# Kernel optimization log

Measured on AMD Instinct MI355X. Metric: run time of the kernel, lower is better.

Reference implementation:

```python
import jax, jax.numpy as jnp
import numpy as np

NUM_STRINGS = 6
WEIGHT_FRET_ONSET = 0.5
STRING_WEIGHTS = jnp.ones((NUM_STRINGS,), dtype=jnp.float32)

B, S, T, C = 64, 6, 2000, 25


def setup_inputs() -> dict:
    key = jax.random.key(0)
    k1, k2, k3, k4 = jax.random.split(key, 4)
    return {
        "output_fret": jax.random.normal(k1, (B, S, T, C), dtype=jnp.float32),
        "target_fret": jax.random.randint(k2, (B, S, T), 0, C),
        "output_onset": jax.random.normal(k3, (B, S, T), dtype=jnp.float32),
        "target_onset": jax.random.uniform(k4, (B, S, T), dtype=jnp.float32),
    }


def reference(output_fret, target_fret, output_onset, target_onset):
    # ---- fret loss: standard CE over classes, mean over batch per (s,t),
    #      summed over frames, weighted per string ----
    logp_fret = jax.nn.log_softmax(output_fret, axis=-1)            # [B,S,T,C]
    nll = -jnp.take_along_axis(logp_fret, target_fret[..., None], axis=-1)[..., 0]  # [B,S,T]
    fret_st = nll.mean(axis=0)                                       # [S,T] (reduction='mean' over batch)
    fret_string_losses = fret_st.sum(axis=1) * STRING_WEIGHTS        # [S]
    fret_loss = fret_string_losses.sum()

    # ---- onset loss: torch CE with 1D [B] input + [B] float target =
    #      single example with B classes and probability targets:
    #      softmax over the BATCH dimension ----
    logp_on = jax.nn.log_softmax(output_onset, axis=0)               # softmax over B
    on_st = -(target_onset * logp_on).sum(axis=0)                    # [S,T]
    onset_string_losses = on_st.sum(axis=1) * STRING_WEIGHTS         # [S]
    onset_loss = onset_string_losses.sum()

    loss = WEIGHT_FRET_ONSET * fret_loss + (1.0 - WEIGHT_FRET_ONSET) * onset_loss
    return (loss, fret_loss, onset_loss, fret_string_losses, onset_string_losses)
```

## Files before the change

### kernel.cpp

```cpp
#include <hip/hip_runtime.h>
#include <math.h>

constexpr int Bn = 64, Sn = 6, Tn = 2000, Cn = 25;
constexpr int COLS = Sn * Tn;
constexpr int ROWS = Bn * Sn * Tn;
constexpr int BDIM = 256;
constexpr int WV   = 4;

constexpr int TROWS = 64;
constexpr int TF4   = TROWS * Cn / 4;
constexpr int NT    = 4;
constexpr int RPW   = NT * TROWS;
constexpr int RPB   = WV * RPW;
constexpr int FBLK  = ROWS / RPB;
constexpr int FPAD  = 768;

constexpr int OCOLS = 64;
constexpr int OBLK  = (COLS + OCOLS - 1) / OCOLS;
constexpr int OPAD  = 192;
constexpr int GRID  = OBLK + FBLK;

typedef const __attribute__((address_space(1))) unsigned int guint;
typedef __attribute__((address_space(3)))       unsigned int luint;

static __device__ __forceinline__ void seg_reduce_add(float* ls, int s, float v, int lane) {
    const int s0 = __shfl(s, 0, 64);
    const int s1 = __shfl(s, 63, 64);
    if (s0 == s1) {
        float a = v;
        #pragma unroll
        for (int off = 32; off; off >>= 1) a += __shfl_xor(a, off, 64);
        if (lane == 0) atomicAdd(&ls[s0], a);
    } else {
        float a = (s == s0) ? v : 0.0f;
        float b = (s == s0) ? 0.0f : v;
        #pragma unroll
        for (int off = 32; off; off >>= 1) {
            a += __shfl_xor(a, off, 64);
            b += __shfl_xor(b, off, 64);
        }
        if (lane == 0) { atomicAdd(&ls[s0], a); atomicAdd(&ls[s1], b); }
    }
}

__global__ __launch_bounds__(BDIM) void main_kernel(const float4* __restrict__ x4,
                                                    const int*    __restrict__ tgt,
                                                    const float*  __restrict__ ox,
                                                    const float*  __restrict__ ot,
                                                    float* __restrict__ pf,
                                                    float* __restrict__ po) {
    __shared__ float4 buf4[WV][2][TF4];
    __shared__ float  ws[WV][Sn];
    const int tid  = threadIdx.x;
    const int lane = tid & 63;
    const int w    = tid >> 6;
    if (lane < Sn) ws[w][lane] = 0.0f;

    if (blockIdx.x < OBLK) {
        const int cb  = blockIdx.x;
        const int col = cb * OCOLS + lane;
        float4* ob4 = &buf4[0][0][0];
        float M = -INFINITY, S = 0.0f, ts = 0.0f, txs = 0.0f;
        if (col < COLS) {
            const int b0 = w * 16;
            #pragma unroll
            for (int h = 0; h < 2; ++h) {
                float xv[8], tv[8];
                #pragma unroll
                for (int k = 0; k < 8; ++k) xv[k] = ox[(b0 + h * 8 + k) * COLS + col];
                #pragma unroll
                for (int k = 0; k < 8; ++k) tv[k] = ot[(b0 + h * 8 + k) * COLS + col];
                float cm = -INFINITY;
                #pragma unroll
                for (int k = 0; k < 8; ++k) cm = fmaxf(cm, xv[k]);
                float cs = 0.0f;
                #pragma unroll
                for (int k = 0; k < 8; ++k) cs += __expf(xv[k] - cm);
                const float nm = fmaxf(M, cm);
                S = S * __expf(M - nm) + cs * __expf(cm - nm);
                M = nm;
                #pragma unroll
                for (int k = 0; k < 8; ++k) { ts += tv[k]; txs += tv[k] * xv[k]; }
            }
        }
        ob4[w * OCOLS + lane] = make_float4(M, S, ts, txs);
        __syncthreads();
        if (tid < OCOLS) {
            float on = 0.0f;
            int   s  = Sn - 1;
            const int c = cb * OCOLS + tid;
            if (c < COLS) {
                s = c / Tn;
                float4 p0 = ob4[0 * OCOLS + tid];
                float Mm = p0.x, Sm = p0.y, tsm = p0.z, txm = p0.w;
                #pragma unroll
                for (int q = 1; q < WV; ++q) {
                    const float4 p = ob4[q * OCOLS + tid];
                    const float nm = fmaxf(Mm, p.x);
                    Sm  = Sm * __expf(Mm - nm) + p.y * __expf(p.x - nm);
                    Mm  = nm;
                    tsm += p.z; txm += p.w;
                }
                on = tsm * (Mm + __logf(Sm)) - txm;
            }
            seg_reduce_add(ws[0], s, on, tid);
            if (tid < Sn) po[tid * OPAD + cb] = ws[0][tid];
        }
    } else {
        const int fb    = blockIdx.x - OBLK;
        const int wrow0 = fb * RPB + w * RPW;
        const float4* gw = x4 + (long)(wrow0 / 4) * Cn;
        float4* bb = &buf4[w][0][0];

        int tcs[NT];
        #pragma unroll
        for (int t = 0; t < NT; ++t) tcs[t] = tgt[wrow0 + t * TROWS + lane];

        auto stage = [&](int t) {
            const int b = t & 1;
            const float4* gs = gw + (long)t * TF4 + lane;
            #pragma unroll
            for (int k = 0; k < 6; ++k)
                __builtin_amdgcn_global_load_lds((guint*)(gs + k * 64),
                                                 (luint*)(bb + b * TF4 + k * 64), 16, 0, 0);
            if (lane < 16)
                __builtin_amdgcn_global_load_lds((guint*)(gs + 384),
                                                 (luint*)(bb + b * TF4 + 384), 16, 0, 0);
        };

        auto compute = [&](int t) {
            const int b  = t & 1;
            const int tc = tcs[t];
            const float* rp = (const float*)(bb + b * TF4) + lane * Cn;
            float m = -INFINITY, xt = 0.0f;
            #pragma unroll
            for (int c = 0; c < Cn; ++c) {
                const float e = rp[c];
                m  = fmaxf(m, e);
                xt = (c == tc) ? e : xt;
            }
            float ss = 0.0f;
            #pragma unroll
            for (int c = 0; c < Cn; ++c) ss += __expf(rp[c] - m);
            const float nll = m + __logf(ss) - xt;
            const int s = ((wrow0 + t * TROWS + lane) / Tn) % Sn;
            seg_reduce_add(ws[w], s, nll, lane);
        };

        stage(0);
        stage(1);
        #pragma unroll
        for (int t = 0; t < NT; ++t) {
            if (t < NT - 1)
                asm volatile("s_waitcnt vmcnt(7)" ::: "memory");
            else
                asm volatile("s_waitcnt vmcnt(0)" ::: "memory");
            compute(t);
            if (t + 2 < NT) {
                asm volatile("s_waitcnt lgkmcnt(0)" ::: "memory");
                stage(t + 2);
            }
        }
        __syncthreads();
        if (tid < Sn)
            pf[tid * FPAD + fb] = ws[0][tid] + ws[1][tid] + ws[2][tid] + ws[3][tid];
    }
}

__global__ __launch_bounds__(1024) void finish_kernel(const float* __restrict__ pf,
                                                      const float* __restrict__ po,
                                                      float* __restrict__ out) {
    __shared__ float acc[2 * Sn];
    const int tid  = threadIdx.x;
    const int lane = tid & 63;
    if (tid < 2 * Sn) acc[tid] = 0.0f;
    __syncthreads();

    float fs[Sn];
    #pragma unroll
    for (int s = 0; s < Sn; ++s) {
        float v = 0.0f;
        for (int i = tid; i < FBLK; i += 1024) v += pf[s * FPAD + i];
        fs[s] = v;
    }
    #pragma unroll
    for (int off = 32; off; off >>= 1) {
        #pragma unroll
        for (int s = 0; s < Sn; ++s) fs[s] += __shfl_xor(fs[s], off, 64);
    }
    if (lane == 0) {
        #pragma unroll
        for (int s = 0; s < Sn; ++s) atomicAdd(&acc[s], fs[s]);
    }

    const int wv = tid >> 6;
    if (wv < Sn) {
        float v = 0.0f;
        for (int i = lane; i < OBLK; i += 64) v += po[wv * OPAD + i];
        #pragma unroll
        for (int off = 32; off; off >>= 1) v += __shfl_xor(v, off, 64);
        if (lane == 0) acc[Sn + wv] = v;
    }
    __syncthreads();

    if (tid == 0) {
        float fret = 0.0f, on = 0.0f, fsv[Sn], osv[Sn];
        #pragma unroll
        for (int s = 0; s < Sn; ++s) {
            fsv[s] = acc[s] * (1.0f / Bn);
            osv[s] = acc[Sn + s];
            fret += fsv[s];
            on   += osv[s];
        }
        out[0] = 0.5f * fret + 0.5f * on;
        out[1] = fret;
        out[2] = on;
        #pragma unroll
        for (int s = 0; s < Sn; ++s) { out[3 + s] = fsv[s]; out[9 + s] = osv[s]; }
    }
}

extern "C" void kernel_launch(void* const* d_in, const int* in_sizes, int n_in,
                              void* d_out, int out_size, void* d_ws, size_t ws_size,
                              hipStream_t stream) {
    const float* output_fret  = (const float*)d_in[0];
    const int*   target_fret  = (const int*)d_in[1];
    const float* output_onset = (const float*)d_in[2];
    const float* target_onset = (const float*)d_in[3];
    float* pf  = (float*)d_ws;
    float* po  = pf + Sn * FPAD;
    float* out = (float*)d_out;

    main_kernel<<<GRID, BDIM, 0, stream>>>((const float4*)output_fret, target_fret,
                                           output_onset, target_onset, pf, po);
    finish_kernel<<<1, 1024, 0, stream>>>(pf, po, out);
}
```

Measured before the change: 25.94 us.

## Fuse finish reduction into main kernel via per-block flags and interleave onset blocks

Removes the second finish kernel launch. An extra last block spins on per-block global completion flags, then reduces the partials and writes the outputs, resetting the flags for the next call. Onset blocks are interleaved among fret blocks (every fifth block) so their work spreads across the grid. The target logit is now read by direct LDS indexing instead of a select inside the loop. The spinning block relies on being scheduled alongside the others and relaxed atomics for visibility, which adds forward-progress and memory-ordering risk.

```diff
diff --git a/kernel.cpp b/kernel.cpp
--- a/kernel.cpp
+++ b/kernel.cpp
@@ -12,16 +12,31 @@
 constexpr int NT    = 4;
 constexpr int RPW   = NT * TROWS;
 constexpr int RPB   = WV * RPW;
-constexpr int FBLK  = ROWS / RPB;
-constexpr int FPAD  = 768;
+constexpr int NFB   = ROWS / RPB;
 
 constexpr int OCOLS = 64;
-constexpr int OBLK  = (COLS + OCOLS - 1) / OCOLS;
-constexpr int OPAD  = 192;
-constexpr int GRID  = OBLK + FBLK;
+constexpr int NOB   = (COLS + OCOLS - 1) / OCOLS;
+constexpr int NBLK  = NFB + NOB;
+constexpr int GRID  = NBLK + 1;
+constexpr int PAD   = 1024;
 
 typedef const __attribute__((address_space(1))) unsigned int guint;
 typedef __attribute__((address_space(3)))       unsigned int luint;
+
+__device__ int g_flag[NBLK];
+
+static __device__ __forceinline__ float agent_loadf(const float* p) {
+    return __hip_atomic_load(p, __ATOMIC_RELAXED, __HIP_MEMORY_SCOPE_AGENT);
+}
+static __device__ __forceinline__ void agent_storef(float* p, float v) {
+    __hip_atomic_store(p, v, __ATOMIC_RELAXED, __HIP_MEMORY_SCOPE_AGENT);
+}
+static __device__ __forceinline__ int agent_loadi(const int* p) {
+    return __hip_atomic_load(p, __ATOMIC_RELAXED, __HIP_MEMORY_SCOPE_AGENT);
+}
+static __device__ __forceinline__ void agent_storei(int* p, int v) {
+    __hip_atomic_store(p, v, __ATOMIC_RELAXED, __HIP_MEMORY_SCOPE_AGENT);
+}
 
 static __device__ __forceinline__ void seg_reduce_add(float* ls, int s, float v, int lane) {
     const int s0 = __shfl(s, 0, 64);
@@ -48,16 +63,77 @@
                                                     const float*  __restrict__ ox,
                                                     const float*  __restrict__ ot,
                                                     float* __restrict__ pf,
-                                                    float* __restrict__ po) {
+                                                    float* __restrict__ po,
+                                                    float* __restrict__ out) {
     __shared__ float4 buf4[WV][2][TF4];
     __shared__ float  ws[WV][Sn];
+    __shared__ float  acc[2 * Sn];
+    __shared__ int    nr;
     const int tid  = threadIdx.x;
     const int lane = tid & 63;
     const int w    = tid >> 6;
+    const int b    = blockIdx.x;
     if (lane < Sn) ws[w][lane] = 0.0f;
 
-    if (blockIdx.x < OBLK) {
-        const int cb  = blockIdx.x;
+    if (b == NBLK) {
+        for (;;) {
+            int ok = 1;
+            for (int i = tid; i < NBLK; i += BDIM) ok &= agent_loadi(&g_flag[i]);
+            if (tid == 0) nr = 0;
+            __syncthreads();
+            if (!ok) nr = 1;
+            __syncthreads();
+            if (nr == 0) break;
+            __builtin_amdgcn_s_sleep(16);
+        }
+        if (tid < 2 * Sn) acc[tid] = 0.0f;
+        __syncthreads();
+        float fs[Sn], os[Sn];
+        #pragma unroll
+        for (int s = 0; s < Sn; ++s) {
+            float v = 0.0f;
+            for (int i = tid; i < NFB; i += BDIM) v += agent_loadf(&pf[s * PAD + i]);
+            fs[s] = v;
+            float u = 0.0f;
+            for (int i = tid; i < NOB; i += BDIM) u += agent_loadf(&po[s * PAD + i]);
+            os[s] = u;
+        }
+        #pragma unroll
+        for (int off = 32; off; off >>= 1) {
+            #pragma unroll
+            for (int s = 0; s < Sn; ++s) {
+                fs[s] += __shfl_xor(fs[s], off, 64);
+                os[s] += __shfl_xor(os[s], off, 64);
+            }
+        }
+        if (lane == 0) {
+            #pragma unroll
+            for (int s = 0; s < Sn; ++s) { atomicAdd(&acc[s], fs[s]); atomicAdd(&acc[Sn + s], os[s]); }
+        }
+        __syncthreads();
+        if (tid == 0) {
+            float fret = 0.0f, on = 0.0f, fsv[Sn], osv[Sn];
+            #pragma unroll
+            for (int s = 0; s < Sn; ++s) {
+                fsv[s] = acc[s] * (1.0f / Bn);
+                osv[s] = acc[Sn + s];
+                fret += fsv[s];
+                on   += osv[s];
+            }
+            out[0] = 0.5f * fret + 0.5f * on;
+            out[1] = fret;
+            out[2] = on;
+            #pragma unroll
+            for (int s = 0; s < Sn; ++s) { out[3 + s] = fsv[s]; out[9 + s] = osv[s]; }
+        }
+        for (int i = tid; i < NBLK; i += BDIM) agent_storei(&g_flag[i], 0);
+        return;
+    }
+
+    const bool isOn = ((b % 5) == 2) && (b / 5 < NOB);
+
+    if (isOn) {
+        const int cb  = b / 5;
         const int col = cb * OCOLS + lane;
         float4* ob4 = &buf4[0][0][0];
         float M = -INFINITY, S = 0.0f, ts = 0.0f, txs = 0.0f;
@@ -104,11 +180,13 @@
                 on = tsm * (Mm + __logf(Sm)) - txm;
             }
             seg_reduce_add(ws[0], s, on, tid);
-            if (tid < Sn) po[tid * OPAD + cb] = ws[0][tid];
+            if (tid < Sn) agent_storef(&po[tid * PAD + cb], ws[0][tid]);
+            asm volatile("s_waitcnt vmcnt(0)" ::: "memory");
+            if (tid == 0) agent_storei(&g_flag[b], 1);
         }
     } else {
-        const int fb    = blockIdx.x - OBLK;
-        const int wrow0 = fb * RPB + w * RPW;
+        const int fid   = b - ((b + 2) / 5 < NOB ? (b + 2) / 5 : NOB);
+        const int wrow0 = fid * RPB + w * RPW;
         const float4* gw = x4 + (long)(wrow0 / 4) * Cn;
         float4* bb = &buf4[w][0][0];
 
@@ -117,28 +195,24 @@
         for (int t = 0; t < NT; ++t) tcs[t] = tgt[wrow0 + t * TROWS + lane];
 
         auto stage = [&](int t) {
-            const int b = t & 1;
+            const int p = t & 1;
             const float4* gs = gw + (long)t * TF4 + lane;
             #pragma unroll
             for (int k = 0; k < 6; ++k)
                 __builtin_amdgcn_global_load_lds((guint*)(gs + k * 64),
-                                                 (luint*)(bb + b * TF4 + k * 64), 16, 0, 0);
+                                                 (luint*)(bb + p * TF4 + k * 64), 16, 0, 0);
             if (lane < 16)
                 __builtin_amdgcn_global_load_lds((guint*)(gs + 384),
-                                                 (luint*)(bb + b * TF4 + 384), 16, 0, 0);
+                                                 (luint*)(bb + p * TF4 + 384), 16, 0, 0);
         };
 
         auto compute = [&](int t) {
-            const int b  = t & 1;
             const int tc = tcs[t];
-            const float* rp = (const float*)(bb + b * TF4) + lane * Cn;
-            float m = -INFINITY, xt = 0.0f;
-            #pragma unroll
-            for (int c = 0; c < Cn; ++c) {
-                const float e = rp[c];
-                m  = fmaxf(m, e);
-                xt = (c == tc) ? e : xt;
-            }
+            const float* rp = (const float*)(bb + (t & 1) * TF4) + lane * Cn;
+            const float xt = rp[tc];
+            float m = -INFINITY;
+            #pragma unroll
+            for (int c = 0; c < Cn; ++c) m = fmaxf(m, rp[c]);
             float ss = 0.0f;
             #pragma unroll
             for (int c = 0; c < Cn; ++c) ss += __expf(rp[c] - m);
@@ -163,60 +237,10 @@
         }
         __syncthreads();
         if (tid < Sn)
-            pf[tid * FPAD + fb] = ws[0][tid] + ws[1][tid] + ws[2][tid] + ws[3][tid];
-    }
-}
-
-__global__ __launch_bounds__(1024) void finish_kernel(const float* __restrict__ pf,
-                                                      const float* __restrict__ po,
-                                                      float* __restrict__ out) {
-    __shared__ float acc[2 * Sn];
-    const int tid  = threadIdx.x;
-    const int lane = tid & 63;
-    if (tid < 2 * Sn) acc[tid] = 0.0f;
-    __syncthreads();
-
-    float fs[Sn];
-    #pragma unroll
-    for (int s = 0; s < Sn; ++s) {
-        float v = 0.0f;
-        for (int i = tid; i < FBLK; i += 1024) v += pf[s * FPAD + i];
-        fs[s] = v;
-    }
-    #pragma unroll
-    for (int off = 32; off; off >>= 1) {
-        #pragma unroll
-        for (int s = 0; s < Sn; ++s) fs[s] += __shfl_xor(fs[s], off, 64);
-    }
-    if (lane == 0) {
-        #pragma unroll
-        for (int s = 0; s < Sn; ++s) atomicAdd(&acc[s], fs[s]);
-    }
-
-    const int wv = tid >> 6;
-    if (wv < Sn) {
-        float v = 0.0f;
-        for (int i = lane; i < OBLK; i += 64) v += po[wv * OPAD + i];
-        #pragma unroll
-        for (int off = 32; off; off >>= 1) v += __shfl_xor(v, off, 64);
-        if (lane == 0) acc[Sn + wv] = v;
-    }
-    __syncthreads();
-
-    if (tid == 0) {
-        float fret = 0.0f, on = 0.0f, fsv[Sn], osv[Sn];
-        #pragma unroll
-        for (int s = 0; s < Sn; ++s) {
-            fsv[s] = acc[s] * (1.0f / Bn);
-            osv[s] = acc[Sn + s];
-            fret += fsv[s];
-            on   += osv[s];
-        }
-        out[0] = 0.5f * fret + 0.5f * on;
-        out[1] = fret;
-        out[2] = on;
-        #pragma unroll
-        for (int s = 0; s < Sn; ++s) { out[3 + s] = fsv[s]; out[9 + s] = osv[s]; }
+            agent_storef(&pf[tid * PAD + fid],
+                         ws[0][tid] + ws[1][tid] + ws[2][tid] + ws[3][tid]);
+        asm volatile("s_waitcnt vmcnt(0)" ::: "memory");
+        if (tid == 0) agent_storei(&g_flag[b], 1);
     }
 }
 
@@ -228,10 +252,9 @@
     const float* output_onset = (const float*)d_in[2];
     const float* target_onset = (const float*)d_in[3];
     float* pf  = (float*)d_ws;
-    float* po  = pf + Sn * FPAD;
+    float* po  = pf + Sn * PAD;
     float* out = (float*)d_out;
 
     main_kernel<<<GRID, BDIM, 0, stream>>>((const float4*)output_fret, target_fret,
-                                           output_onset, target_onset, pf, po);
-    finish_kernel<<<1, 1024, 0, stream>>>(pf, po, out);
-}
+                                           output_onset, target_onset, pf, po, out);
+}
```

New measurement: 31.20 us. 20.3% more time.

## Replace static fret tile assignment with atomic per-channel dynamic work queues

Applied to the files above, without the earlier changes.

Fret blocks no longer take a fixed slice of four tiles per wave. Each wave now grabs pairs of 64-row tiles from one of eight atomic counters in global memory, which should balance load and shorten the tail. Target indices are now fetched asynchronously into LDS next to the logits instead of being preloaded into registers. The cost is an atomic round-trip per grab, a data-dependent loop in place of a fully unrolled one, and counters that the finish kernel must reset for the next launch.

```diff
diff --git a/kernel.cpp b/kernel.cpp
--- a/kernel.cpp
+++ b/kernel.cpp
@@ -9,19 +9,21 @@
 
 constexpr int TROWS = 64;
 constexpr int TF4   = TROWS * Cn / 4;
-constexpr int NT    = 4;
-constexpr int RPW   = NT * TROWS;
-constexpr int RPB   = WV * RPW;
-constexpr int FBLK  = ROWS / RPB;
-constexpr int FPAD  = 768;
+constexpr int NTIL  = ROWS / TROWS;
+constexpr int NC    = 8;
+constexpr int TPC   = NTIL / NC;
+constexpr int Q     = 2;
 
 constexpr int OCOLS = 64;
 constexpr int OBLK  = (COLS + OCOLS - 1) / OCOLS;
-constexpr int OPAD  = 192;
-constexpr int GRID  = OBLK + FBLK;
+constexpr int NFB   = 768;
+constexpr int GRID  = OBLK + NFB;
+constexpr int PAD   = 1024;
 
 typedef const __attribute__((address_space(1))) unsigned int guint;
 typedef __attribute__((address_space(3)))       unsigned int luint;
+
+__device__ int qctr[NC];
 
 static __device__ __forceinline__ void seg_reduce_add(float* ls, int s, float v, int lane) {
     const int s0 = __shfl(s, 0, 64);
@@ -50,14 +52,16 @@
                                                     float* __restrict__ pf,
                                                     float* __restrict__ po) {
     __shared__ float4 buf4[WV][2][TF4];
+    __shared__ int    tbuf[WV][2][TROWS];
     __shared__ float  ws[WV][Sn];
     const int tid  = threadIdx.x;
     const int lane = tid & 63;
     const int w    = tid >> 6;
+    const int b    = blockIdx.x;
     if (lane < Sn) ws[w][lane] = 0.0f;
 
-    if (blockIdx.x < OBLK) {
-        const int cb  = blockIdx.x;
+    if (b < OBLK) {
+        const int cb  = b;
         const int col = cb * OCOLS + lane;
         float4* ob4 = &buf4[0][0][0];
         float M = -INFINITY, S = 0.0f, ts = 0.0f, txs = 0.0f;
@@ -104,66 +108,79 @@
                 on = tsm * (Mm + __logf(Sm)) - txm;
             }
             seg_reduce_add(ws[0], s, on, tid);
-            if (tid < Sn) po[tid * OPAD + cb] = ws[0][tid];
+            if (tid < Sn) po[tid * PAD + cb] = ws[0][tid];
         }
     } else {
-        const int fb    = blockIdx.x - OBLK;
-        const int wrow0 = fb * RPB + w * RPW;
-        const float4* gw = x4 + (long)(wrow0 / 4) * Cn;
+        const int fb = b - OBLK;
+        const int c  = (fb * WV + w) & (NC - 1);
         float4* bb = &buf4[w][0][0];
 
-        int tcs[NT];
-        #pragma unroll
-        for (int t = 0; t < NT; ++t) tcs[t] = tgt[wrow0 + t * TROWS + lane];
-
-        auto stage = [&](int t) {
-            const int b = t & 1;
-            const float4* gs = gw + (long)t * TF4 + lane;
+        int base = 0, lim = 0;
+        auto next_tile = [&]() -> int {
+            if (base >= lim) {
+                int idx = 0;
+                if (lane == 0) idx = atomicAdd(&qctr[c], 1);
+                idx  = __shfl(idx, 0, 64);
+                base = idx * Q;
+                lim  = base + Q;
+            }
+            if (base >= TPC) return -1;
+            return base++;
+        };
+
+        auto stage = [&](int lt, int p) {
+            const int gt = c * TPC + lt;
+            const float4* gs = x4 + (long)gt * TF4 + lane;
             #pragma unroll
             for (int k = 0; k < 6; ++k)
                 __builtin_amdgcn_global_load_lds((guint*)(gs + k * 64),
-                                                 (luint*)(bb + b * TF4 + k * 64), 16, 0, 0);
+                                                 (luint*)(bb + p * TF4 + k * 64), 16, 0, 0);
             if (lane < 16)
                 __builtin_amdgcn_global_load_lds((guint*)(gs + 384),
-                                                 (luint*)(bb + b * TF4 + 384), 16, 0, 0);
+                                                 (luint*)(bb + p * TF4 + 384), 16, 0, 0);
+            __builtin_amdgcn_global_load_lds((guint*)(tgt + (long)gt * TROWS + lane),
+                                             (luint*)&tbuf[w][p][0], 4, 0, 0);
         };
 
-        auto compute = [&](int t) {
-            const int b  = t & 1;
-            const int tc = tcs[t];
-            const float* rp = (const float*)(bb + b * TF4) + lane * Cn;
+        auto compute = [&](int lt, int p) {
+            const int gt = c * TPC + lt;
+            const int tc = tbuf[w][p][lane];
+            const float* rp = (const float*)(bb + p * TF4) + lane * Cn;
             float m = -INFINITY, xt = 0.0f;
             #pragma unroll
-            for (int c = 0; c < Cn; ++c) {
-                const float e = rp[c];
+            for (int cc = 0; cc < Cn; ++cc) {
+                const float e = rp[cc];
                 m  = fmaxf(m, e);
-                xt = (c == tc) ? e : xt;
+                xt = (cc == tc) ? e : xt;
             }
             float ss = 0.0f;
             #pragma unroll
-            for (int c = 0; c < Cn; ++c) ss += __expf(rp[c] - m);
+            for (int cc = 0; cc < Cn; ++cc) ss += __expf(rp[cc] - m);
             const float nll = m + __logf(ss) - xt;
-            const int s = ((wrow0 + t * TROWS + lane) / Tn) % Sn;
+            const int s = ((gt * TROWS + lane) / Tn) % Sn;
             seg_reduce_add(ws[w], s, nll, lane);
         };
 
-        stage(0);
-        stage(1);
-        #pragma unroll
-        for (int t = 0; t < NT; ++t) {
-            if (t < NT - 1)
-                asm volatile("s_waitcnt vmcnt(7)" ::: "memory");
-            else
-                asm volatile("s_waitcnt vmcnt(0)" ::: "memory");
-            compute(t);
-            if (t + 2 < NT) {
+        int t0 = next_tile();
+        if (t0 >= 0) stage(t0, 0);
+        int t1 = next_tile();
+        if (t1 >= 0) stage(t1, 1);
+        int p = 0;
+        while (t0 >= 0) {
+            if (t1 >= 0) asm volatile("s_waitcnt vmcnt(8)" ::: "memory");
+            else         asm volatile("s_waitcnt vmcnt(0)" ::: "memory");
+            compute(t0, p);
+            int t2 = -1;
+            if (t1 >= 0) t2 = next_tile();
+            if (t2 >= 0) {
                 asm volatile("s_waitcnt lgkmcnt(0)" ::: "memory");
-                stage(t + 2);
-            }
+                stage(t2, p);
+            }
+            t0 = t1; t1 = t2; p ^= 1;
         }
         __syncthreads();
         if (tid < Sn)
-            pf[tid * FPAD + fb] = ws[0][tid] + ws[1][tid] + ws[2][tid] + ws[3][tid];
+            pf[tid * PAD + fb] = ws[0][tid] + ws[1][tid] + ws[2][tid] + ws[3][tid];
     }
 }
 
@@ -173,33 +190,38 @@
     __shared__ float acc[2 * Sn];
     const int tid  = threadIdx.x;
     const int lane = tid & 63;
+    if (tid < NC) qctr[tid] = 0;
     if (tid < 2 * Sn) acc[tid] = 0.0f;
     __syncthreads();
 
-    float fs[Sn];
+    float fs[Sn], os[Sn];
     #pragma unroll
     for (int s = 0; s < Sn; ++s) {
-        float v = 0.0f;
-        for (int i = tid; i < FBLK; i += 1024) v += pf[s * FPAD + i];
-        fs[s] = v;
-    }
-    #pragma unroll
-    for (int off = 32; off; off >>= 1) {
-        #pragma unroll
-        for (int s = 0; s < Sn; ++s) fs[s] += __shfl_xor(fs[s], off, 64);
-    }
-    if (lane == 0) {
-        #pragma unroll
-        for (int s = 0; s < Sn; ++s) atomicAdd(&acc[s], fs[s]);
-    }
-
+        fs[s] = (tid < NFB) ? pf[s * PAD + tid] : 0.0f;
+        float u = 0.0f;
+        for (int i = lane; i < OBLK; i += 64) u += 0.0f;
+        os[s] = 0.0f;
+    }
     const int wv = tid >> 6;
     if (wv < Sn) {
         float v = 0.0f;
-        for (int i = lane; i < OBLK; i += 64) v += po[wv * OPAD + i];
+        for (int i = lane; i < OBLK; i += 64) v += po[wv * PAD + i];
+        os[wv] = v;
+    }
+    #pragma unroll
+    for (int off = 32; off; off >>= 1) {
+        #pragma unroll
+        for (int s = 0; s < Sn; ++s) fs[s] += __shfl_xor(fs[s], off, 64);
+    }
+    if (wv < Sn) {
+        float v = os[wv];
         #pragma unroll
         for (int off = 32; off; off >>= 1) v += __shfl_xor(v, off, 64);
         if (lane == 0) acc[Sn + wv] = v;
+    }
+    if (lane == 0) {
+        #pragma unroll
+        for (int s = 0; s < Sn; ++s) atomicAdd(&acc[s], fs[s]);
     }
     __syncthreads();
 
@@ -228,7 +250,7 @@
     const float* output_onset = (const float*)d_in[2];
     const float* target_onset = (const float*)d_in[3];
     float* pf  = (float*)d_ws;
-    float* po  = pf + Sn * FPAD;
+    float* po  = pf + Sn * PAD;
     float* out = (float*)d_out;
 
     main_kernel<<<GRID, BDIM, 0, stream>>>((const float4*)output_fret, target_fret,
```

Result: slower. 67.67 us (+160.8%).
